# Kernel tuning notes

Measured on AMD Instinct MI355X. Metric: run time of the kernel, lower is better.

The kernel has to match this reference:

```python
import jax, jax.numpy as jnp
import numpy as np


def setup_inputs() -> dict:
    key = jax.random.key(0)
    ks = jax.random.split(key, 5)
    B, S, D, L = 16, 256, 768, 32
    return {
        "head": jax.random.normal(ks[0], (B, S, D), dtype=jnp.float32),
        "dep": jax.random.normal(ks[1], (B, S, D), dtype=jnp.float32),
        "label_U_diag": jax.random.normal(ks[2], (L, D), dtype=jnp.float32) * 0.02,
        "label_W": jax.random.normal(ks[3], (L, 2 * D), dtype=jnp.float32) * 0.02,
        "label_b": jax.random.normal(ks[4], (L,), dtype=jnp.float32) * 0.02,
    }


def reference(head, dep, label_U_diag, label_W, label_b):
    # head, dep: [b, s, d]; label_U_diag: [l, d]; label_W: [l, 2d]; label_b: [l]
    d = head.shape[-1]
    # Bilinear term with diagonal U: t1[b,l,i,o] = sum_d head[b,i,d]*U[l,d]*dep[b,o,d]
    t1 = jnp.einsum('bid,ld,bod->blio', head, label_U_diag, dep)
    # Linear term: W @ concat(head_i, dep_o) = W_h @ head_i + W_d @ dep_o
    W_h, W_d = label_W[:, :d], label_W[:, d:]
    t2_h = jnp.einsum('ld,bid->bli', W_h, head)  # [b, l, s]
    t2_d = jnp.einsum('ld,bod->blo', W_d, dep)   # [b, l, s]
    return t1 + t2_h[:, :, :, None] + t2_d[:, :, None, :] + label_b[None, :, None, None]
```

## Files before the change

### kernel.cpp

```cpp
#include <hip/hip_runtime.h>
#include <hip/hip_bf16.h>
#include <stdint.h>


#define B_ 16
#define S_ 256
#define D_ 768
#define L_ 32
#define KQ_ (D_ / 8)
#define NT_ 12
#define NC_ 24

typedef unsigned short ushort_t;
typedef __attribute__((ext_vector_type(4))) float f32x4;
typedef __attribute__((ext_vector_type(8))) short s16x8;

__device__ __forceinline__ unsigned int pack_bf16(float f0, float f1) {
  unsigned int u0 = __builtin_bit_cast(unsigned int, f0) + 0x8000u;
  unsigned int u1 = __builtin_bit_cast(unsigned int, f1) + 0x8000u;
  return __builtin_amdgcn_perm(u1, u0, 0x07060302);
}

__global__ __launch_bounds__(256) void prep_kernel(
    const float* __restrict__ head, const float* __restrict__ dep,
    const float* __restrict__ labelW, ushort_t* __restrict__ depb,
    float* __restrict__ t2h, float* __restrict__ t2d) {
  const int wave = threadIdx.x >> 6;
  const int lane = threadIdx.x & 63;
  const int g = blockIdx.x * 4 + wave;
  const int sel = g >> 10;
  const int idx = g & 1023;
  const int b = idx >> 6;
  const int row0 = (idx & 63) * 4;
  const float* src = sel ? dep : head;
  float* t2x = sel ? t2d : t2h;
  const int d0 = lane * 12;

  float h[4][12];
  const float* rp = src + ((size_t)(b * S_ + row0)) * D_ + d0;
#pragma unroll
  for (int r = 0; r < 4; ++r) {
    float4 v0 = *(const float4*)(rp + (size_t)r * D_);
    float4 v1 = *(const float4*)(rp + (size_t)r * D_ + 4);
    float4 v2 = *(const float4*)(rp + (size_t)r * D_ + 8);
    h[r][0] = v0.x; h[r][1] = v0.y; h[r][2] = v0.z; h[r][3] = v0.w;
    h[r][4] = v1.x; h[r][5] = v1.y; h[r][6] = v1.z; h[r][7] = v1.w;
    h[r][8] = v2.x; h[r][9] = v2.y; h[r][10] = v2.z; h[r][11] = v2.w;
  }
  if (sel) {
    const size_t bb = (size_t)b * (KQ_ * S_ * 8);
    const int m = lane >> 1;
#pragma unroll
    for (int r = 0; r < 4; ++r) {
      const int col = row0 + r;
      unsigned int q0 = pack_bf16(h[r][0], h[r][1]);
      unsigned int q1 = pack_bf16(h[r][2], h[r][3]);
      unsigned int q2 = pack_bf16(h[r][4], h[r][5]);
      unsigned int q3 = pack_bf16(h[r][6], h[r][7]);
      unsigned int q4 = pack_bf16(h[r][8], h[r][9]);
      unsigned int q5 = pack_bf16(h[r][10], h[r][11]);
      if ((lane & 1) == 0) {
        uint4 a = {q0, q1, q2, q3};
        uint2 c = {q4, q5};
        *(uint4*)(depb + bb + ((size_t)(3 * m) * S_ + col) * 8) = a;
        *(uint2*)(depb + bb + ((size_t)(3 * m + 1) * S_ + col) * 8) = c;
      } else {
        uint2 c = {q0, q1};
        uint4 a = {q2, q3, q4, q5};
        *(uint2*)(depb + bb + ((size_t)(3 * m + 1) * S_ + col) * 8 + 4) = c;
        *(uint4*)(depb + bb + ((size_t)(3 * m + 2) * S_ + col) * 8) = a;
      }
    }
  }
  const float* wbase = labelW + sel * D_ + d0;
  for (int c = 0; c < 2; ++c) {
    float v[64];
#pragma unroll
    for (int j = 0; j < 64; ++j) v[j] = 0.f;
    const float* wc = wbase + (size_t)(c * 16) * (2 * D_);
#pragma unroll
    for (int lq = 0; lq < 16; ++lq) {
      const float* wp = wc + (size_t)lq * (2 * D_);
      float4 w0 = *(const float4*)(wp);
      float4 w1 = *(const float4*)(wp + 4);
      float4 w2 = *(const float4*)(wp + 8);
      float w[12] = {w0.x, w0.y, w0.z, w0.w, w1.x, w1.y, w1.z, w1.w,
                     w2.x, w2.y, w2.z, w2.w};
#pragma unroll
      for (int j = 0; j < 12; ++j) {
        v[lq * 4 + 0] += h[0][j] * w[j];
        v[lq * 4 + 1] += h[1][j] * w[j];
        v[lq * 4 + 2] += h[2][j] * w[j];
        v[lq * 4 + 3] += h[3][j] * w[j];
      }
    }
#pragma unroll
    for (int off = 32; off >= 1; off >>= 1) {
      const bool hi = (lane & off) != 0;
#pragma unroll
      for (int k = 0; k < 64; ++k) {
        if (k >= off) continue;
        float send = hi ? v[k] : v[k + off];
        float keep = hi ? v[k + off] : v[k];
        v[k] = keep + __shfl_xor(send, off);
      }
    }
    t2x[((size_t)(b * L_ + c * 16 + (lane >> 2))) * S_ + row0 + (lane & 3)] =
        v[0];
  }
}


#define SWZ(o) ((o) ^ ((((o) >> 10) & 3) << 4))

__global__ __launch_bounds__(256, 2) void main_kernel(
    const float* __restrict__ head, const ushort_t* __restrict__ depb,
    const float* __restrict__ U, const float* __restrict__ bias,
    const float* __restrict__ t2h, const float* __restrict__ t2d,
    float* __restrict__ out) {
  __shared__ __attribute__((aligned(16))) ushort_t As[2 * 2 * 4096];
  __shared__ float T2[384];

  const int hw = blockIdx.x;
  const int bid = ((hw & 7) << 7) | (hw >> 3);
  const int ic = bid & 1;
  const int bl = bid >> 1;
  const int l = bl & (L_ - 1);
  const int b = bl >> 5;
  const int ti = ic * 128;
  const int t = threadIdx.x;
  const int lane = t & 63;
  const int wave = t >> 6;
  const int wr = wave >> 1;
  const int wc = wave & 1;

  for (int i = t; i < 384; i += 256)
    T2[i] = (i < 128) ? t2h[((size_t)(b * L_ + l)) * S_ + ti + i]
                      : t2d[((size_t)(b * L_ + l)) * S_ + (i - 128)];
  const float bv = bias[l];

  const int row0 = t >> 2;
  const int kg = t & 3;
  const float* hp0 = head + ((size_t)(b * S_ + ti + row0)) * D_ + kg * 8;
  const float* hp1 = hp0 + (size_t)64 * D_;
  const float* Up = U + (size_t)l * D_ + kg * 8;
  const int awo0s = SWZ((kg * 128 + row0) * 8);
  const int awo1s = awo0s + 512;

  const int aros = SWZ(((lane >> 4) * 128 + (lane & 15)) * 8) + wr * 512;

  const ushort_t* dfb =
      depb + (size_t)b * (KQ_ * S_ * 8) +
      ((size_t)((lane >> 4) * 256 + wc * 128 + (lane & 15))) * 8;

  f32x4 acc[4][8];
#pragma unroll
  for (int i = 0; i < 4; ++i)
#pragma unroll
    for (int j = 0; j < 8; ++j) acc[i][j] = {0.f, 0.f, 0.f, 0.f};

  s16x8 bfA[8], bfB[8];

#define LOAD_HU(ku)                                                           \
    float4 h0 = *(const float4*)(hp0 + (ku) * 32);                            \
    float4 h1 = *(const float4*)(hp0 + (ku) * 32 + 4);                        \
    float4 h2 = *(const float4*)(hp1 + (ku) * 32);                            \
    float4 h3 = *(const float4*)(hp1 + (ku) * 32 + 4);                        \
    float4 u0 = *(const float4*)(Up + (ku) * 32);                             \
    float4 u1 = *(const float4*)(Up + (ku) * 32 + 4);

#define PACK_WRITE_A(DST)                                                     \
  {                                                                           \
    uint4 w0, w1;                                                             \
    w0.x = pack_bf16(h0.x * u0.x, h0.y * u0.y);                               \
    w0.y = pack_bf16(h0.z * u0.z, h0.w * u0.w);                               \
    w0.z = pack_bf16(h1.x * u1.x, h1.y * u1.y);                               \
    w0.w = pack_bf16(h1.z * u1.z, h1.w * u1.w);                               \
    w1.x = pack_bf16(h2.x * u0.x, h2.y * u0.y);                               \
    w1.y = pack_bf16(h2.z * u0.z, h2.w * u0.w);                               \
    w1.z = pack_bf16(h3.x * u1.x, h3.y * u1.y);                               \
    w1.w = pack_bf16(h3.z * u1.z, h3.w * u1.w);                               \
    *(uint4*)((DST) + awo0s) = w0;                                            \
    *(uint4*)((DST) + awo1s) = w1;                                            \
  }

#define LOAD_BF(DSTB, chunk)                                                  \
  {                                                                           \
    const ushort_t* dfn = dfb + (size_t)(chunk) * 8192;                       \
    _Pragma("unroll") for (int ct = 0; ct < 8; ++ct)                          \
        DSTB[ct] = *(const s16x8*)(dfn + ct * 128);                           \
  }

#define MFMA16(AFB, BFB)                                                      \
  {                                                                           \
    _Pragma("unroll") for (int rt = 0; rt < 4; ++rt)                          \
      _Pragma("unroll") for (int ct = 0; ct < 8; ++ct)                        \
          acc[rt][ct] = __builtin_amdgcn_mfma_f32_16x16x32_bf16(              \
              AFB[rt], BFB[ct], acc[rt][ct], 0, 0, 0);                        \
  }

  {
    {
      LOAD_HU(0)
      PACK_WRITE_A(As)
    }
    {
      LOAD_HU(1)
      PACK_WRITE_A(As + 4096)
    }
    LOAD_BF(bfA, 0)
  }
  asm volatile("s_waitcnt lgkmcnt(0)" ::: "memory");
  __builtin_amdgcn_s_barrier();
  __builtin_amdgcn_sched_barrier(0);

  int cur = 0;
  for (int tt = 0; tt < NT_; ++tt) {
    const ushort_t* pr = As + cur * 8192;
    ushort_t* pw = As + (cur ^ 1) * 8192;
    {
      LOAD_BF(bfB, 2 * tt + 1)
      int ks = 2 * tt + 2;
      if (ks >= NC_) ks -= NC_;
      LOAD_HU(ks)
      __builtin_amdgcn_sched_barrier(0);
      s16x8 af[4];
#pragma unroll
      for (int rt = 0; rt < 4; ++rt)
        af[rt] = *(const s16x8*)(pr + aros + rt * 128);
      __builtin_amdgcn_s_setprio(1);
      MFMA16(af, bfA)
      __builtin_amdgcn_s_setprio(0);
      PACK_WRITE_A(pw)
    }
    {
      int cb = 2 * tt + 2;
      if (cb >= NC_) cb -= NC_;
      LOAD_BF(bfA, cb)
      int ks = 2 * tt + 3;
      if (ks >= NC_) ks -= NC_;
      LOAD_HU(ks)
      __builtin_amdgcn_sched_barrier(0);
      s16x8 af[4];
#pragma unroll
      for (int rt = 0; rt < 4; ++rt)
        af[rt] = *(const s16x8*)(pr + 4096 + aros + rt * 128);
      __builtin_amdgcn_s_setprio(1);
      MFMA16(af, bfB)
      __builtin_amdgcn_s_setprio(0);
      PACK_WRITE_A(pw + 4096)
    }
    asm volatile("s_waitcnt lgkmcnt(0)" ::: "memory");
    __builtin_amdgcn_s_barrier();
    __builtin_amdgcn_sched_barrier(0);
    cur ^= 1;
  }
#undef LOAD_HU
#undef PACK_WRITE_A
#undef LOAD_BF
#undef MFMA16

  const int colg = lane & 15;
  const int rgrp = lane >> 4;
  float* ob = out + (((size_t)(b * L_ + l)) * S_ + ti + wr * 64) * S_ + wc * 128;
#pragma unroll
  for (int rt = 0; rt < 4; ++rt) {
    const int r0 = rt * 16 + rgrp * 4;
#pragma unroll
    for (int ct = 0; ct < 8; ++ct) {
      const int c = ct * 16 + colg;
      const float addc = T2[128 + wc * 128 + c] + bv;
      float* p = ob + (size_t)r0 * S_ + c;
#pragma unroll
      for (int r = 0; r < 4; ++r)
        p[(size_t)r * S_] = acc[rt][ct][r] + T2[wr * 64 + r0 + r] + addc;
    }
  }
}

extern "C" void kernel_launch(void* const* d_in, const int* in_sizes, int n_in,
                              void* d_out, int out_size, void* d_ws, size_t ws_size,
                              hipStream_t stream) {
  const float* head = (const float*)d_in[0];
  const float* dep = (const float*)d_in[1];
  const float* U = (const float*)d_in[2];
  const float* W = (const float*)d_in[3];
  const float* bias = (const float*)d_in[4];
  float* out = (float*)d_out;

  ushort_t* depb = (ushort_t*)d_ws;
  float* t2h = (float*)((char*)d_ws + (size_t)B_ * S_ * D_ * 2);
  float* t2d = t2h + (size_t)B_ * L_ * S_;

  prep_kernel<<<512, 256, 0, stream>>>(head, dep, W, depb, t2h, t2d);
  main_kernel<<<B_ * L_ * 2, 256, 0, stream>>>(head, depb, U, bias, t2h, t2d, out);
}
```

Baseline: 224.1 us.

## Shrink LDS double buffer to single k-chunk and split B fragment prefetch

Restructures the main loop to process one k-chunk per barrier instead of two, halving the LDS A-tile buffer to two 4096-element stages. B fragments are split into low and high halves, and the high half is loaded after the MFMAs that consume it. This cuts register and LDS footprint, which may allow more waves per CU. The cost is twice as many barriers per block and a shorter prefetch distance for the B operand, which can expose more load latency.

```diff
diff --git a/kernel.cpp b/kernel.cpp
--- a/kernel.cpp
+++ b/kernel.cpp
@@ -8,7 +8,6 @@
 #define D_ 768
 #define L_ 32
 #define KQ_ (D_ / 8)
-#define NT_ 12
 #define NC_ 24
 
 typedef unsigned short ushort_t;
@@ -118,7 +117,7 @@
     const float* __restrict__ U, const float* __restrict__ bias,
     const float* __restrict__ t2h, const float* __restrict__ t2d,
     float* __restrict__ out) {
-  __shared__ __attribute__((aligned(16))) ushort_t As[2 * 2 * 4096];
+  __shared__ __attribute__((aligned(16))) ushort_t As[2 * 4096];
   __shared__ float T2[384];
 
   const int hw = blockIdx.x;
@@ -159,7 +158,8 @@
 #pragma unroll
     for (int j = 0; j < 8; ++j) acc[i][j] = {0.f, 0.f, 0.f, 0.f};
 
-  s16x8 bfA[8], bfB[8];
+  s16x8 bfA[4], bfB[4];
+  s16x8 bfHi[4];
 
 #define LOAD_HU(ku)                                                           \
     float4 h0 = *(const float4*)(hp0 + (ku) * 32);                            \
@@ -184,81 +184,63 @@
     *(uint4*)((DST) + awo1s) = w1;                                            \
   }
 
-#define LOAD_BF(DSTB, chunk)                                                  \
+#define LOAD_BF4(DSTB, chunk, off)                                            \
   {                                                                           \
     const ushort_t* dfn = dfb + (size_t)(chunk) * 8192;                       \
-    _Pragma("unroll") for (int ct = 0; ct < 8; ++ct)                          \
-        DSTB[ct] = *(const s16x8*)(dfn + ct * 128);                           \
-  }
-
-#define MFMA16(AFB, BFB)                                                      \
+    _Pragma("unroll") for (int ct = 0; ct < 4; ++ct)                          \
+        DSTB[ct] = *(const s16x8*)(dfn + ((off) + ct) * 128);                 \
+  }
+
+#define MFMA8(AFB, BFB, CO)                                                   \
   {                                                                           \
     _Pragma("unroll") for (int rt = 0; rt < 4; ++rt)                          \
-      _Pragma("unroll") for (int ct = 0; ct < 8; ++ct)                        \
-          acc[rt][ct] = __builtin_amdgcn_mfma_f32_16x16x32_bf16(              \
-              AFB[rt], BFB[ct], acc[rt][ct], 0, 0, 0);                        \
+      _Pragma("unroll") for (int ct = 0; ct < 4; ++ct)                        \
+          acc[rt][(CO) + ct] = __builtin_amdgcn_mfma_f32_16x16x32_bf16(       \
+              AFB[rt], BFB[ct], acc[rt][(CO) + ct], 0, 0, 0);                 \
   }
 
   {
-    {
-      LOAD_HU(0)
-      PACK_WRITE_A(As)
-    }
-    {
-      LOAD_HU(1)
-      PACK_WRITE_A(As + 4096)
-    }
-    LOAD_BF(bfA, 0)
+    LOAD_HU(0)
+    PACK_WRITE_A(As)
+    LOAD_BF4(bfA, 0, 0)
+    LOAD_BF4(bfHi, 0, 4)
   }
   asm volatile("s_waitcnt lgkmcnt(0)" ::: "memory");
   __builtin_amdgcn_s_barrier();
   __builtin_amdgcn_sched_barrier(0);
 
-  int cur = 0;
-  for (int tt = 0; tt < NT_; ++tt) {
-    const ushort_t* pr = As + cur * 8192;
-    ushort_t* pw = As + (cur ^ 1) * 8192;
-    {
-      LOAD_BF(bfB, 2 * tt + 1)
-      int ks = 2 * tt + 2;
-      if (ks >= NC_) ks -= NC_;
-      LOAD_HU(ks)
-      __builtin_amdgcn_sched_barrier(0);
-      s16x8 af[4];
-#pragma unroll
-      for (int rt = 0; rt < 4; ++rt)
-        af[rt] = *(const s16x8*)(pr + aros + rt * 128);
-      __builtin_amdgcn_s_setprio(1);
-      MFMA16(af, bfA)
-      __builtin_amdgcn_s_setprio(0);
-      PACK_WRITE_A(pw)
-    }
-    {
-      int cb = 2 * tt + 2;
-      if (cb >= NC_) cb -= NC_;
-      LOAD_BF(bfA, cb)
-      int ks = 2 * tt + 3;
-      if (ks >= NC_) ks -= NC_;
-      LOAD_HU(ks)
-      __builtin_amdgcn_sched_barrier(0);
-      s16x8 af[4];
-#pragma unroll
-      for (int rt = 0; rt < 4; ++rt)
-        af[rt] = *(const s16x8*)(pr + 4096 + aros + rt * 128);
-      __builtin_amdgcn_s_setprio(1);
-      MFMA16(af, bfB)
-      __builtin_amdgcn_s_setprio(0);
-      PACK_WRITE_A(pw + 4096)
-    }
-    asm volatile("s_waitcnt lgkmcnt(0)" ::: "memory");
-    __builtin_amdgcn_s_barrier();
-    __builtin_amdgcn_sched_barrier(0);
-    cur ^= 1;
-  }
+#define ITER(PB, BLC, BLN, tcur)                                              \
+  {                                                                           \
+    int tn = (tcur) + 1;                                                      \
+    if (tn == NC_) tn = 0;     \
+    LOAD_BF4(BLN, tn, 0)                                                      \
+    LOAD_HU(tn)                                                               \
+    __builtin_amdgcn_sched_barrier(0);       \
+    const ushort_t* pr = As + (PB)*4096;                                      \
+    s16x8 af[4];                                                              \
+    _Pragma("unroll") for (int rt = 0; rt < 4; ++rt)                          \
+        af[rt] = *(const s16x8*)(pr + aros + rt * 128);                       \
+    __builtin_amdgcn_s_setprio(1);                                            \
+    MFMA8(af, BLC, 0)                                                         \
+    MFMA8(af, bfHi, 4)                                                        \
+    __builtin_amdgcn_s_setprio(0);                                            \
+    __builtin_amdgcn_sched_barrier(0);      \
+    LOAD_BF4(bfHi, tn, 4)                                                     \
+    PACK_WRITE_A(As + ((PB) ^ 1) * 4096)                                      \
+    asm volatile("s_waitcnt lgkmcnt(0)" ::: "memory");                        \
+    __builtin_amdgcn_s_barrier();                                             \
+    __builtin_amdgcn_sched_barrier(0);                                        \
+  }
+
+  for (int tt = 0; tt < NC_; tt += 2) {
+    ITER(0, bfA, bfB, tt)
+    ITER(1, bfB, bfA, tt + 1)
+  }
+#undef ITER
 #undef LOAD_HU
 #undef PACK_WRITE_A
-#undef LOAD_BF
-#undef MFMA16
+#undef LOAD_BF4
+#undef MFMA8
 
   const int colg = lane & 15;
   const int rgrp = lane >> 4;
```

New measurement: 219.6 us. 2.0% less time.
